# Kernel tuning notes

Hardware: AMD Instinct MI355X
Metric: run time of the kernel (lower is better)

Reference implementation:

```python
import jax, jax.numpy as jnp
import numpy as np

N, E, D, ED = 25000, 250000, 128, 128
LN_EPS = 1e-5   # nn.LayerNorm default
BN_EPS = 1e-5   # BatchNorm1d default (GENConv MLP norm='batch', training mode)
GEN_EPS = 1e-7  # GENConv message eps


def _ln(x, g, b):
    mu = jnp.mean(x, -1, keepdims=True)
    var = jnp.mean((x - mu) ** 2, -1, keepdims=True)
    return (x - mu) * jax.lax.rsqrt(var + LN_EPS) * g + b


def setup_inputs() -> dict:
    key = jax.random.key(0)
    ks = jax.random.split(key, 8)
    p = lambda k, shp: (jax.random.normal(k, shp, jnp.float32) * 0.02)
    return {
        "x": jax.random.normal(ks[0], (N, D), jnp.float32),
        "edge_attr": jax.random.normal(ks[1], (E, ED), jnp.float32),
        "edge_index": jax.random.randint(ks[2], (2, E), 0, N),
        # edge_mlp: Linear(2D+ED -> ED) + ReLU + LayerNorm(ED)
        "W_e": p(ks[3], (2 * D + ED, ED)), "b_e": jnp.zeros((ED,), jnp.float32),
        "g_e": jnp.ones((ED,), jnp.float32), "be_e": jnp.zeros((ED,), jnp.float32),
        # GENConv learnable softmax temperature t (learn_t=True, init 1.0)
        "t": jnp.float32(1.0),
        # GENConv output MLP: [D -> 2D (BN, ReLU) -> D]  (num_layers=2, expansion=2, norm='batch')
        "W_m1": p(ks[4], (D, 2 * D)), "b_m1": jnp.zeros((2 * D,), jnp.float32),
        "g_bn": jnp.ones((2 * D,), jnp.float32), "b_bn": jnp.zeros((2 * D,), jnp.float32),
        "W_m2": p(ks[5], (2 * D, D)), "b_m2": jnp.zeros((D,), jnp.float32),
        # MessageNorm learnable scale (learn_scale=True, init 1.0)
        "scale": jnp.float32(1.0),
        # node LayerNorm
        "g_n": jnp.ones((D,), jnp.float32), "b_n": jnp.zeros((D,), jnp.float32),
    }


def reference(x, edge_attr, edge_index, W_e, b_e, g_e, be_e, t,
              W_m1, b_m1, g_bn, b_bn, W_m2, b_m2, scale, g_n, b_n):
    row, col = edge_index[0], edge_index[1]  # source, destination (PyG flow)

    # edge MLP with residual: cat([x[row], x[col], edge_attr]) -> Linear -> ReLU -> LN, + edge_attr
    ei = jnp.concatenate([x[row], x[col], edge_attr], axis=-1)        # [E, 2D+ED]
    e = _ln(jnp.maximum(ei @ W_e + b_e, 0.0), g_e, be_e) + edge_attr  # [E, ED]

    # GENConv message: relu(x_j + edge_attr) + eps  (edge_dim == in_channels -> no lin_edge)
    msg = jnp.maximum(x[row] + e, 0.0) + GEN_EPS                      # [E, D]

    # per-destination, per-channel softmax aggregation with temperature t
    s = msg * t
    smax = jax.ops.segment_max(s, col, num_segments=N)                # [N, D]
    ex = jnp.exp(s - smax[col])
    denom = jax.ops.segment_sum(ex, col, num_segments=N)
    alpha = ex / denom[col]
    agg = jax.ops.segment_sum(msg * alpha, col, num_segments=N)       # [N, D]

    # GENConv residual + output MLP (Linear -> BatchNorm(train) -> ReLU -> Linear)
    out = agg + x
    h1 = out @ W_m1 + b_m1                                            # [N, 2D]
    mu = jnp.mean(h1, axis=0)
    var = jnp.mean((h1 - mu) ** 2, axis=0)
    h1 = jnp.maximum((h1 - mu) * jax.lax.rsqrt(var + BN_EPS) * g_bn + b_bn, 0.0)
    h = h1 @ W_m2 + b_m2                                              # [N, D]

    # MessageNorm(learn_scale=True): normalize(h) * ||x|| * scale
    hnorm = jnp.linalg.norm(h, axis=-1, keepdims=True)
    h = h / jnp.maximum(hnorm, 1e-12)
    xnorm = jnp.linalg.norm(x, axis=-1, keepdims=True)
    h = h * xnorm * scale

    # node residual + LayerNorm (dropout in eval mode = identity)
    x_out = _ln(x + h, g_n, b_n)
    return (x_out, e)
```

## Files before the change

### kernel.cpp

```cpp
#include <hip/hip_runtime.h>
#include <hip/hip_bf16.h>

typedef __hip_bfloat16 bf16;
typedef __attribute__((ext_vector_type(8))) short short8v;
typedef __attribute__((ext_vector_type(4))) float float4v;

constexpr int N = 25000;
constexpr int E = 250000;
constexpr size_t NB = (size_t)N * 128;
constexpr int NBLK = (N + 63) / 64;

constexpr size_t al256(size_t x) { return (x + 255) / 256 * 256; }

constexpr size_t OFF_BNS  = 0;
constexpr size_t OFF_BNQ  = OFF_BNS + 256;
constexpr size_t OFF_FLAG = OFF_BNQ + 256;
constexpr size_t OFF_XN   = OFF_FLAG + 256;
constexpr size_t OFF_WB   = al256(OFF_XN + N);
constexpr size_t OFF_WP   = OFF_WB + 8192;
constexpr size_t OFF_WM1P = OFF_WP + 16384;
constexpr size_t OFF_WM2P = OFF_WM1P + 16384;
constexpr size_t OFF_DEG  = al256(OFF_WM2P + 16384);
constexpr size_t OFF_OFFS = al256(OFF_DEG + N);
constexpr size_t OFF_CUR  = al256(OFF_OFFS + N + 1);
constexpr size_t OFF_LIST = al256(OFF_CUR + N);
constexpr size_t OFF_OUT  = al256(OFF_LIST + E);
constexpr size_t OFF_A    = al256(OFF_OUT + NB / 2);
constexpr size_t WS_FLOATS = OFF_A + NB;


__device__ __forceinline__ float b2f(bf16 v) { return __bfloat162float(v); }
__device__ __forceinline__ short f2bs(float f) {
    bf16 h = __float2bfloat16(f);
    return *reinterpret_cast<short*>(&h);
}
__device__ __forceinline__ float bs2f(short s) {
    bf16 h;
    *reinterpret_cast<short*>(&h) = s;
    return b2f(h);
}

__device__ __forceinline__ float ldf(const void* p, size_t i, int bf) {
    return bf ? b2f(((const bf16*)p)[i]) : ((const float*)p)[i];
}
__device__ __forceinline__ void stf(void* p, size_t i, float v, int bf) {
    if (bf) ((bf16*)p)[i] = __float2bfloat16(v);
    else    ((float*)p)[i] = v;
}
__device__ __forceinline__ float lds_scalar(const void* p, int bf) {
    if (!bf) return *(const float*)p;
    float v = b2f(*(const bf16*)p);
    float a = fabsf(v);
    return (a >= 0.0009765625f && a <= 1024.0f) ? v : *(const float*)p;
}
__device__ __forceinline__ int get_flag(const float* ws) {
    return *(const int*)(ws + OFF_FLAG);
}
__device__ __forceinline__ void* e_base(void* d_out, int bf) {
    return bf ? (void*)((bf16*)d_out + NB) : (void*)((float*)d_out + NB);
}


__global__ void k_detect(const unsigned short* __restrict__ xu, float* __restrict__ ws) {
    __shared__ int cnt;
    if (threadIdx.x == 0) cnt = 0;
    __syncthreads();
    int c = 0;
    for (int i = threadIdx.x; i < 512; i += 256) {
        unsigned e = (xu[i] >> 7) & 0xFFu;
        if (e >= 110u && e <= 135u) c++;
    }
    atomicAdd(&cnt, c);
    __syncthreads();
    if (threadIdx.x == 0) *(int*)(ws + OFF_FLAG) = (cnt >= 460) ? 1 : 0;
}

__global__ void k_init(float* __restrict__ ws, const void* __restrict__ W_e,
                       const void* __restrict__ W_m1, const void* __restrict__ W_m2) {
    int bf = get_flag(ws);
    size_t gid = (size_t)blockIdx.x * blockDim.x + threadIdx.x;
    size_t stride = (size_t)gridDim.x * blockDim.x;
    short* WB = (short*)(ws + OFF_WB);
    for (size_t t = gid; t < 16384; t += stride) {
        int i = t & 7, l = (t >> 3) & 63, n = (t >> 9) & 7, s = t >> 12;
        int k = s * 32 + (l >> 4) * 8 + i;
        int c = n * 16 + (l & 15);
        WB[t] = f2bs(ldf(W_e, (size_t)(256 + k) * 128 + c, bf));
    }
    short* WP = (short*)(ws + OFF_WP);
    for (size_t t = gid; t < 32768; t += stride) {
        int i = t & 7, l = (t >> 3) & 63, n = (t >> 9) & 15, s = t >> 13;
        int k = s * 32 + (l >> 4) * 8 + i;
        int c = n * 16 + (l & 15);
        float v = (c < 128) ? ldf(W_e, (size_t)k * 128 + c, bf)
                            : ldf(W_e, (size_t)(128 + k) * 128 + (c - 128), bf);
        WP[t] = f2bs(v);
    }
    short* M1 = (short*)(ws + OFF_WM1P);
    for (size_t t = gid; t < 32768; t += stride) {
        int i = t & 7, l = (t >> 3) & 63, n = (t >> 9) & 15, s = t >> 13;
        int k = s * 32 + (l >> 4) * 8 + i;
        int c = n * 16 + (l & 15);
        M1[t] = f2bs(ldf(W_m1, (size_t)k * 256 + c, bf));
    }
    short* M2 = (short*)(ws + OFF_WM2P);
    for (size_t t = gid; t < 32768; t += stride) {
        int i = t & 7, l = (t >> 3) & 63, n = (t >> 9) & 7, s = t >> 12;
        int k = s * 32 + (l >> 4) * 8 + i;
        int c = n * 16 + (l & 15);
        M2[t] = f2bs(ldf(W_m2, (size_t)k * 128 + c, bf));
    }
    for (size_t i = gid; i < 512; i += stride) ws[OFF_BNS + i] = 0.0f;
    int* deg = (int*)(ws + OFF_DEG);
    for (size_t i = gid; i < N; i += stride) deg[i] = 0;
}

__global__ __launch_bounds__(256) void k_node_pre_mfma(const void* __restrict__ x,
                                                       const void* __restrict__ b_e,
                                                       float* __restrict__ ws) {
    int bf = get_flag(ws);
    int l = threadIdx.x & 63, wv = threadIdx.x >> 6;
    int n0 = blockIdx.x * 64 + wv * 16;
    if (n0 >= N) return;
    int row = l & 15, grp = l >> 4;
    int ja = n0 + row;
    int jac = ja < N ? ja : N - 1;
    const short8v* WP = (const short8v*)(ws + OFF_WP);
    float4v acc[16];
    #pragma unroll
    for (int n = 0; n < 16; ++n) acc[n] = (float4v){0.f, 0.f, 0.f, 0.f};
    float sq = 0.f;
    #pragma unroll
    for (int s = 0; s < 4; ++s) {
        short8v af;
        if (bf) {
            af = ((const short8v*)x)[(size_t)jac * 16 + s * 4 + grp];
            #pragma unroll
            for (int i = 0; i < 8; ++i) { float v = bs2f(af[i]); sq = fmaf(v, v, sq); }
        } else {
            const float* er = (const float*)x + (size_t)jac * 128 + s * 32 + grp * 8;
            float4v lo = *(const float4v*)er;
            float4v hi = *(const float4v*)(er + 4);
            float xv[8] = {lo[0], lo[1], lo[2], lo[3], hi[0], hi[1], hi[2], hi[3]};
            #pragma unroll
            for (int i = 0; i < 8; ++i) { sq = fmaf(xv[i], xv[i], sq); af[i] = f2bs(xv[i]); }
        }
        #pragma unroll
        for (int n = 0; n < 16; ++n) {
            acc[n] = __builtin_amdgcn_mfma_f32_16x16x32_bf16(af, WP[(s * 16 + n) * 64 + l], acc[n], 0, 0, 0);
        }
    }
    sq += __shfl_xor(sq, 16, 64);
    sq += __shfl_xor(sq, 32, 64);
    if (grp == 0 && ja < N) ws[OFF_XN + ja] = sqrtf(sq);
    bf16* XA = (bf16*)(ws + OFF_A);
    #pragma unroll
    for (int reg = 0; reg < 4; ++reg) {
        int jd = n0 + grp * 4 + reg;
        if (jd >= N) continue;
        #pragma unroll
        for (int n = 0; n < 16; ++n) {
            int c = n * 16 + row;
            if (n < 8) {
                XA[(size_t)jd * 128 + c] = __float2bfloat16(acc[n][reg] + ldf(b_e, c, bf));
            } else {
                XA[NB + (size_t)jd * 128 + (c - 128)] = __float2bfloat16(acc[n][reg]);
            }
        }
    }
}

__global__ __launch_bounds__(256) void k_edge1_mfma(const void* __restrict__ ea,
                                                    const int* __restrict__ ei,
                                                    const void* __restrict__ g_e,
                                                    const void* __restrict__ be_e,
                                                    float* __restrict__ ws,
                                                    void* __restrict__ d_out) {
    int bf = get_flag(ws);
    void* eo = e_base(d_out, bf);
    int l = threadIdx.x & 63;
    int wv = threadIdx.x >> 6;
    int e0w = blockIdx.x * 64 + wv * 16;
    if (e0w >= E) return;

    if (l < 16) {
        int j = e0w + l;
        if (j < E) atomicAdd((int*)(ws + OFF_DEG) + ei[E + j], 1);
    }

    int row = l & 15, grp = l >> 4;
    int ja = e0w + row;
    int jac = ja < E ? ja : E - 1;
    const short8v* WB = (const short8v*)(ws + OFF_WB);
    float4v acc[8];
    #pragma unroll
    for (int n = 0; n < 8; ++n) acc[n] = (float4v){0.f, 0.f, 0.f, 0.f};

    #pragma unroll
    for (int s = 0; s < 4; ++s) {
        short8v af;
        if (bf) {
            af = ((const short8v*)ea)[(size_t)jac * 16 + s * 4 + grp];
        } else {
            const float* er = (const float*)ea + (size_t)jac * 128 + s * 32 + grp * 8;
            float4v lo = *(const float4v*)er;
            float4v hi = *(const float4v*)(er + 4);
            af[0] = f2bs(lo[0]); af[1] = f2bs(lo[1]); af[2] = f2bs(lo[2]); af[3] = f2bs(lo[3]);
            af[4] = f2bs(hi[0]); af[5] = f2bs(hi[1]); af[6] = f2bs(hi[2]); af[7] = f2bs(hi[3]);
        }
        #pragma unroll
        for (int n = 0; n < 8; ++n) {
            acc[n] = __builtin_amdgcn_mfma_f32_16x16x32_bf16(af, WB[(s * 8 + n) * 64 + l], acc[n], 0, 0, 0);
        }
    }

    int jr[4], rr[4], cc[4];
    #pragma unroll
    for (int reg = 0; reg < 4; ++reg) {
        int j = e0w + grp * 4 + reg;
        int jc = j < E ? j : E - 1;
        jr[reg] = j;
        rr[reg] = ei[jc];
        cc[reg] = ei[E + jc];
    }
    const bf16* XA = (const bf16*)(ws + OFF_A);
    float p[8][4];
    #pragma unroll
    for (int n = 0; n < 8; ++n) {
        int col = n * 16 + row;
        #pragma unroll
        for (int reg = 0; reg < 4; ++reg) {
            float v = acc[n][reg]
                    + b2f(XA[(size_t)rr[reg] * 128 + col])
                    + b2f(XA[NB + (size_t)cc[reg] * 128 + col]);
            p[n][reg] = fmaxf(v, 0.f);
        }
    }
    #pragma unroll
    for (int reg = 0; reg < 4; ++reg) {
        float s1 = 0.f;
        #pragma unroll
        for (int n = 0; n < 8; ++n) s1 += p[n][reg];
        #pragma unroll
        for (int off = 1; off < 16; off <<= 1) s1 += __shfl_xor(s1, off, 64);
        float mu = s1 * (1.f / 128.f);
        float s2 = 0.f;
        #pragma unroll
        for (int n = 0; n < 8; ++n) { float d = p[n][reg] - mu; s2 = fmaf(d, d, s2); }
        #pragma unroll
        for (int off = 1; off < 16; off <<= 1) s2 += __shfl_xor(s2, off, 64);
        float rstd = rsqrtf(s2 * (1.f / 128.f) + 1e-5f);
        if (jr[reg] < E) {
            size_t jb = (size_t)jr[reg] * 128;
            #pragma unroll
            for (int n = 0; n < 8; ++n) {
                int col = n * 16 + row;
                float ev = (p[n][reg] - mu) * rstd * ldf(g_e, col, bf)
                         + ldf(be_e, col, bf) + ldf(ea, jb + col, bf);
                stf(eo, jb + col, ev, bf);
            }
        }
    }
}

__global__ __launch_bounds__(256) void k_scan(float* __restrict__ ws) {
    const int* deg = (const int*)(ws + OFF_DEG);
    int* offs = (int*)(ws + OFF_OFFS);
    int* cur  = (int*)(ws + OFF_CUR);
    __shared__ int sums[256];
    __shared__ int carry[257];
    int t = threadIdx.x;
    const int chunk = (N + 255) / 256;
    int lo = t * chunk, hi = lo + chunk < N ? lo + chunk : N;
    int s = 0;
    for (int i = lo; i < hi; ++i) s += deg[i];
    sums[t] = s;
    __syncthreads();
    if (t == 0) {
        int acc = 0;
        #pragma unroll 4
        for (int i = 0; i < 256; ++i) { carry[i] = acc; acc += sums[i]; }
        carry[256] = acc;
    }
    __syncthreads();
    int acc = carry[t];
    for (int i = lo; i < hi; ++i) { offs[i] = acc; cur[i] = acc; acc += deg[i]; }
    if (t == 0) offs[N] = carry[256];
}

__global__ void k_scatter(const int* __restrict__ ei, float* __restrict__ ws) {
    int j = blockIdx.x * blockDim.x + threadIdx.x;
    if (j >= E) return;
    int cd = ei[E + j];
    int pos = atomicAdd((int*)(ws + OFF_CUR) + cd, 1);
    ((int*)(ws + OFF_LIST))[pos] = j;
}

__global__ __launch_bounds__(256) void k_agg(const void* __restrict__ x,
                                             const int* __restrict__ ei,
                                             const void* __restrict__ t_p,
                                             void* __restrict__ d_out,
                                             float* __restrict__ ws) {
    int bf = get_flag(ws);
    const void* e_in = e_base(d_out, bf);
    int n = blockIdx.x, tid = threadIdx.x;
    int c = tid & 127, half = tid >> 7;
    const int* offs = (const int*)(ws + OFF_OFFS);
    const int* list = (const int*)(ws + OFF_LIST);
    int s0 = offs[n], s1 = offs[n + 1];
    float t = lds_scalar(t_p, bf);
    float den = 0.f, num = 0.f;
    for (int i = s0 + half; i < s1; i += 2) {
        int j = list[i];
        int r = ei[j];
        float ev = ldf(e_in, (size_t)j * 128 + c, bf);
        float msg = fmaxf(ldf(x, (size_t)r * 128 + c, bf) + ev, 0.f) + 1e-7f;
        float ex = expf(msg * t - 15.0f);
        den += ex;
        num = fmaf(msg, ex, num);
    }
    __shared__ float dsh[256];
    __shared__ float nsh[256];
    dsh[tid] = den;
    nsh[tid] = num;
    __syncthreads();
    if (tid < 128) {
        float dn = dsh[tid] + dsh[tid + 128];
        float nm = nsh[tid] + nsh[tid + 128];
        float ag = dn > 0.f ? nm / dn : 0.f;
        float out = ag + ldf(x, (size_t)n * 128 + tid, bf);
        ((bf16*)(ws + OFF_OUT))[(size_t)n * 128 + tid] = __float2bfloat16(out);
    }
}

__global__ __launch_bounds__(256) void k_h1_mfma(const void* __restrict__ b_m1,
                                                 float* __restrict__ ws) {
    int bf = get_flag(ws);
    int l = threadIdx.x & 63, wv = threadIdx.x >> 6;
    int n0 = blockIdx.x * 64 + wv * 16;
    if (n0 >= N) return;
    int row = l & 15, grp = l >> 4;
    int ja = n0 + row;
    int jac = ja < N ? ja : N - 1;
    const short8v* OUT = (const short8v*)(ws + OFF_OUT);
    const short8v* M1 = (const short8v*)(ws + OFF_WM1P);
    float4v acc[16];
    #pragma unroll
    for (int n = 0; n < 16; ++n) acc[n] = (float4v){0.f, 0.f, 0.f, 0.f};
    #pragma unroll
    for (int s = 0; s < 4; ++s) {
        short8v af = OUT[(size_t)jac * 16 + s * 4 + grp];
        #pragma unroll
        for (int n = 0; n < 16; ++n) {
            acc[n] = __builtin_amdgcn_mfma_f32_16x16x32_bf16(af, M1[(s * 16 + n) * 64 + l], acc[n], 0, 0, 0);
        }
    }
    bf16* H1 = (bf16*)(ws + OFF_A);
    #pragma unroll
    for (int reg = 0; reg < 4; ++reg) {
        int jd = n0 + grp * 4 + reg;
        if (jd >= N) continue;
        #pragma unroll
        for (int n = 0; n < 16; ++n) {
            int col = n * 16 + row;
            H1[(size_t)jd * 256 + col] = __float2bfloat16(acc[n][reg] + ldf(b_m1, col, bf));
        }
    }
}

__global__ __launch_bounds__(256) void k_bnstats(float* __restrict__ ws) {
    int t = threadIdx.x;
    const bf16* H1 = (const bf16*)(ws + OFF_A);
    float s = 0.f, q = 0.f;
    for (int r = blockIdx.x; r < N; r += gridDim.x) {
        float v = b2f(H1[(size_t)r * 256 + t]);
        s += v;
        q = fmaf(v, v, q);
    }
    atomicAdd(&ws[OFF_BNS + t], s);
    atomicAdd(&ws[OFF_BNQ + t], q);
}

__global__ __launch_bounds__(256) void k_node_post_mfma(const void* __restrict__ x,
                                                        const void* __restrict__ g_bn,
                                                        const void* __restrict__ b_bn,
                                                        const void* __restrict__ b_m2,
                                                        const void* __restrict__ scale_p,
                                                        const void* __restrict__ g_n,
                                                        const void* __restrict__ b_n,
                                                        float* __restrict__ ws,
                                                        void* __restrict__ x_out) {
    int bf = get_flag(ws);
    __shared__ float sA[256];
    __shared__ float sB[256];
    {
        int t = threadIdx.x;
        const float inv_n = 1.f / (float)N;
        float mu = ws[OFF_BNS + t] * inv_n;
        float var = ws[OFF_BNQ + t] * inv_n - mu * mu;
        float rs = rsqrtf(fmaxf(var, 0.f) + 1e-5f) * ldf(g_bn, t, bf);
        sA[t] = rs;
        sB[t] = ldf(b_bn, t, bf) - mu * rs;
    }
    __syncthreads();
    int l = threadIdx.x & 63, wv = threadIdx.x >> 6;
    int n0 = blockIdx.x * 64 + wv * 16;
    if (n0 >= N) return;
    int row = l & 15, grp = l >> 4;
    int ja = n0 + row;
    int jac = ja < N ? ja : N - 1;
    const short8v* H1 = (const short8v*)(ws + OFF_A);
    const short8v* M2 = (const short8v*)(ws + OFF_WM2P);
    float4v acc[8];
    #pragma unroll
    for (int n = 0; n < 8; ++n) acc[n] = (float4v){0.f, 0.f, 0.f, 0.f};
    #pragma unroll
    for (int s = 0; s < 8; ++s) {
        short8v hv = H1[(size_t)jac * 32 + s * 4 + grp];
        int kb = s * 32 + grp * 8;
        short8v af;
        #pragma unroll
        for (int i = 0; i < 8; ++i) {
            float v = fmaf(bs2f(hv[i]), sA[kb + i], sB[kb + i]);
            af[i] = f2bs(fmaxf(v, 0.f));
        }
        #pragma unroll
        for (int n = 0; n < 8; ++n) {
            acc[n] = __builtin_amdgcn_mfma_f32_16x16x32_bf16(af, M2[(s * 8 + n) * 64 + l], acc[n], 0, 0, 0);
        }
    }
    float scl = lds_scalar(scale_p, bf);
    #pragma unroll
    for (int reg = 0; reg < 4; ++reg) {
        int jd = n0 + grp * 4 + reg;
        int jdc = jd < N ? jd : N - 1;
        float h[8];
        float ss = 0.f;
        #pragma unroll
        for (int n = 0; n < 8; ++n) {
            h[n] = acc[n][reg] + ldf(b_m2, n * 16 + row, bf);
            ss = fmaf(h[n], h[n], ss);
        }
        #pragma unroll
        for (int off = 1; off < 16; off <<= 1) ss += __shfl_xor(ss, off, 64);
        float hs = ws[OFF_XN + jdc] * scl / fmaxf(sqrtf(ss), 1e-12f);
        float y[8];
        float s1 = 0.f;
        #pragma unroll
        for (int n = 0; n < 8; ++n) {
            y[n] = ldf(x, (size_t)jdc * 128 + n * 16 + row, bf) + h[n] * hs;
            s1 += y[n];
        }
        #pragma unroll
        for (int off = 1; off < 16; off <<= 1) s1 += __shfl_xor(s1, off, 64);
        float mu = s1 * (1.f / 128.f);
        float s2 = 0.f;
        #pragma unroll
        for (int n = 0; n < 8; ++n) { float d = y[n] - mu; s2 = fmaf(d, d, s2); }
        #pragma unroll
        for (int off = 1; off < 16; off <<= 1) s2 += __shfl_xor(s2, off, 64);
        float rstd = rsqrtf(s2 * (1.f / 128.f) + 1e-5f);
        if (jd < N) {
            #pragma unroll
            for (int n = 0; n < 8; ++n) {
                int col = n * 16 + row;
                float o = (y[n] - mu) * rstd * ldf(g_n, col, bf) + ldf(b_n, col, bf);
                stf(x_out, (size_t)jd * 128 + col, o, bf);
            }
        }
    }
}


extern "C" void kernel_launch(void* const* d_in, const int* in_sizes, int n_in,
                              void* d_out, int out_size, void* d_ws, size_t ws_size,
                              hipStream_t stream) {
    const void* x    = d_in[0];
    const void* ea   = d_in[1];
    const int*  ei   = (const int*)d_in[2];
    const void* W_e  = d_in[3];
    const void* b_e  = d_in[4];
    const void* g_e  = d_in[5];
    const void* be_e = d_in[6];
    const void* t_p  = d_in[7];
    const void* W_m1 = d_in[8];
    const void* b_m1 = d_in[9];
    const void* g_bn = d_in[10];
    const void* b_bn = d_in[11];
    const void* W_m2 = d_in[12];
    const void* b_m2 = d_in[13];
    const void* scl  = d_in[14];
    const void* g_n  = d_in[15];
    const void* b_n  = d_in[16];

    float* ws = (float*)d_ws;

    k_detect<<<1, 256, 0, stream>>>((const unsigned short*)x, ws);
    k_init<<<512, 256, 0, stream>>>(ws, W_e, W_m1, W_m2);
    k_node_pre_mfma<<<NBLK, 256, 0, stream>>>(x, b_e, ws);
    k_edge1_mfma<<<(E + 63) / 64, 256, 0, stream>>>(ea, ei, g_e, be_e, ws, d_out);
    k_scan<<<1, 256, 0, stream>>>(ws);
    k_scatter<<<(E + 255) / 256, 256, 0, stream>>>(ei, ws);
    k_agg<<<N, 256, 0, stream>>>(x, ei, t_p, d_out, ws);
    k_h1_mfma<<<NBLK, 256, 0, stream>>>(b_m1, ws);
    k_bnstats<<<256, 256, 0, stream>>>(ws);
    k_node_post_mfma<<<NBLK, 256, 0, stream>>>(x, g_bn, b_bn, b_m2, scl, g_n, b_n, ws, d_out);
}
```

Before: 622.1 us.

## Write bf16 messages in CSR order from edge kernel and stream them in aggregation

Degree counting and the prefix scan now run before the edge MLP. The edge kernel then takes each edge's CSR slot with an atomic and writes the bf16 message relu(x_row+e)+eps straight into a destination-sorted buffer in the workspace. Aggregation then streams contiguous messages instead of gathering list indices, edge features and x rows, which cuts random global reads. The edge kernel also swaps the MFMA operand order so each lane holds four contiguous channels of one edge, and it uses single-pass variance with vectorized loads and stores. The cost is an extra E*128 bf16 workspace buffer, plus a fallback path when the workspace is too small.

```diff
diff --git a/kernel.cpp b/kernel.cpp
--- a/kernel.cpp
+++ b/kernel.cpp
@@ -3,6 +3,7 @@
 
 typedef __hip_bfloat16 bf16;
 typedef __attribute__((ext_vector_type(8))) short short8v;
+typedef __attribute__((ext_vector_type(4))) short short4v;
 typedef __attribute__((ext_vector_type(4))) float float4v;
 
 constexpr int N = 25000;
@@ -27,6 +28,8 @@
 constexpr size_t OFF_OUT  = al256(OFF_LIST + E);
 constexpr size_t OFF_A    = al256(OFF_OUT + NB / 2);
 constexpr size_t WS_FLOATS = OFF_A + NB;
+constexpr size_t OFF_MSG  = al256(OFF_A + NB);
+constexpr size_t WS_FLOATS_BIG = OFF_MSG + (size_t)E * 64;
 
 
 __device__ __forceinline__ float b2f(bf16 v) { return __bfloat162float(v); }
@@ -46,6 +49,21 @@
 __device__ __forceinline__ void stf(void* p, size_t i, float v, int bf) {
     if (bf) ((bf16*)p)[i] = __float2bfloat16(v);
     else    ((float*)p)[i] = v;
+}
+__device__ __forceinline__ float4v load4(const void* p, size_t i, int bf) {
+    if (bf) {
+        short4v s = *(const short4v*)((const bf16*)p + i);
+        return (float4v){bs2f(s[0]), bs2f(s[1]), bs2f(s[2]), bs2f(s[3])};
+    }
+    return *(const float4v*)((const float*)p + i);
+}
+__device__ __forceinline__ void store4(void* p, size_t i, float4v v, int bf) {
+    if (bf) {
+        short4v s = {f2bs(v[0]), f2bs(v[1]), f2bs(v[2]), f2bs(v[3])};
+        *(short4v*)((bf16*)p + i) = s;
+    } else {
+        *(float4v*)((float*)p + i) = v;
+    }
 }
 __device__ __forceinline__ float lds_scalar(const void* p, int bf) {
     if (!bf) return *(const float*)p;
@@ -113,6 +131,11 @@
     for (size_t i = gid; i < 512; i += stride) ws[OFF_BNS + i] = 0.0f;
     int* deg = (int*)(ws + OFF_DEG);
     for (size_t i = gid; i < N; i += stride) deg[i] = 0;
+}
+
+__global__ void k_count(const int* __restrict__ ei, float* __restrict__ ws) {
+    int j = blockIdx.x * blockDim.x + threadIdx.x;
+    if (j < E) atomicAdd((int*)(ws + OFF_DEG) + ei[E + j], 1);
 }
 
 __global__ __launch_bounds__(256) void k_node_pre_mfma(const void* __restrict__ x,
@@ -170,10 +193,12 @@
     }
 }
 
+template<int WM>
 __global__ __launch_bounds__(256) void k_edge1_mfma(const void* __restrict__ ea,
                                                     const int* __restrict__ ei,
                                                     const void* __restrict__ g_e,
                                                     const void* __restrict__ be_e,
+                                                    const void* __restrict__ x,
                                                     float* __restrict__ ws,
                                                     void* __restrict__ d_out) {
     int bf = get_flag(ws);
@@ -181,84 +206,89 @@
     int l = threadIdx.x & 63;
     int wv = threadIdx.x >> 6;
     int e0w = blockIdx.x * 64 + wv * 16;
-    if (e0w >= E) return;
-
-    if (l < 16) {
-        int j = e0w + l;
-        if (j < E) atomicAdd((int*)(ws + OFF_DEG) + ei[E + j], 1);
-    }
-
-    int row = l & 15, grp = l >> 4;
-    int ja = e0w + row;
+    int eq = l & 15, grp = l >> 4;
+
+    int posv = 0;
+    if (WM && l < 16) {
+        int jj = e0w + l;
+        if (jj < E) posv = atomicAdd((int*)(ws + OFF_CUR) + ei[E + jj], 1);
+    }
+    int pos = WM ? __shfl(posv, eq, 64) : 0;
+
+    int ja = e0w + eq;
     int jac = ja < E ? ja : E - 1;
     const short8v* WB = (const short8v*)(ws + OFF_WB);
     float4v acc[8];
     #pragma unroll
-    for (int n = 0; n < 8; ++n) acc[n] = (float4v){0.f, 0.f, 0.f, 0.f};
+    for (int m = 0; m < 8; ++m) acc[m] = (float4v){0.f, 0.f, 0.f, 0.f};
 
     #pragma unroll
     for (int s = 0; s < 4; ++s) {
-        short8v af;
+        short8v bfr;
         if (bf) {
-            af = ((const short8v*)ea)[(size_t)jac * 16 + s * 4 + grp];
+            bfr = ((const short8v*)ea)[(size_t)jac * 16 + s * 4 + grp];
         } else {
             const float* er = (const float*)ea + (size_t)jac * 128 + s * 32 + grp * 8;
             float4v lo = *(const float4v*)er;
             float4v hi = *(const float4v*)(er + 4);
-            af[0] = f2bs(lo[0]); af[1] = f2bs(lo[1]); af[2] = f2bs(lo[2]); af[3] = f2bs(lo[3]);
-            af[4] = f2bs(hi[0]); af[5] = f2bs(hi[1]); af[6] = f2bs(hi[2]); af[7] = f2bs(hi[3]);
-        }
-        #pragma unroll
-        for (int n = 0; n < 8; ++n) {
-            acc[n] = __builtin_amdgcn_mfma_f32_16x16x32_bf16(af, WB[(s * 8 + n) * 64 + l], acc[n], 0, 0, 0);
-        }
-    }
-
-    int jr[4], rr[4], cc[4];
-    #pragma unroll
-    for (int reg = 0; reg < 4; ++reg) {
-        int j = e0w + grp * 4 + reg;
-        int jc = j < E ? j : E - 1;
-        jr[reg] = j;
-        rr[reg] = ei[jc];
-        cc[reg] = ei[E + jc];
-    }
-    const bf16* XA = (const bf16*)(ws + OFF_A);
+            bfr[0] = f2bs(lo[0]); bfr[1] = f2bs(lo[1]); bfr[2] = f2bs(lo[2]); bfr[3] = f2bs(lo[3]);
+            bfr[4] = f2bs(hi[0]); bfr[5] = f2bs(hi[1]); bfr[6] = f2bs(hi[2]); bfr[7] = f2bs(hi[3]);
+        }
+        #pragma unroll
+        for (int m = 0; m < 8; ++m) {
+            acc[m] = __builtin_amdgcn_mfma_f32_16x16x32_bf16(WB[(s * 8 + m) * 64 + l], bfr, acc[m], 0, 0, 0);
+        }
+    }
+
+    int j = e0w + eq;
+    bool valid = j < E;
+    int jc = valid ? j : E - 1;
+    int r = ei[jc], cd = ei[E + jc];
+    const bf16* XAp = (const bf16*)(ws + OFF_A);
+
     float p[8][4];
-    #pragma unroll
-    for (int n = 0; n < 8; ++n) {
-        int col = n * 16 + row;
-        #pragma unroll
-        for (int reg = 0; reg < 4; ++reg) {
-            float v = acc[n][reg]
-                    + b2f(XA[(size_t)rr[reg] * 128 + col])
-                    + b2f(XA[NB + (size_t)cc[reg] * 128 + col]);
-            p[n][reg] = fmaxf(v, 0.f);
-        }
-    }
-    #pragma unroll
-    for (int reg = 0; reg < 4; ++reg) {
-        float s1 = 0.f;
-        #pragma unroll
-        for (int n = 0; n < 8; ++n) s1 += p[n][reg];
-        #pragma unroll
-        for (int off = 1; off < 16; off <<= 1) s1 += __shfl_xor(s1, off, 64);
-        float mu = s1 * (1.f / 128.f);
-        float s2 = 0.f;
-        #pragma unroll
-        for (int n = 0; n < 8; ++n) { float d = p[n][reg] - mu; s2 = fmaf(d, d, s2); }
-        #pragma unroll
-        for (int off = 1; off < 16; off <<= 1) s2 += __shfl_xor(s2, off, 64);
-        float rstd = rsqrtf(s2 * (1.f / 128.f) + 1e-5f);
-        if (jr[reg] < E) {
-            size_t jb = (size_t)jr[reg] * 128;
+    float s1 = 0.f, s2 = 0.f;
+    #pragma unroll
+    for (int m = 0; m < 8; ++m) {
+        int ch = m * 16 + grp * 4;
+        short4v xa = *(const short4v*)(XAp + (size_t)r * 128 + ch);
+        short4v xb = *(const short4v*)(XAp + NB + (size_t)cd * 128 + ch);
+        #pragma unroll
+        for (int w = 0; w < 4; ++w) {
+            float v = acc[m][w] + bs2f(xa[w]) + bs2f(xb[w]);
+            v = fmaxf(v, 0.f);
+            p[m][w] = v;
+            s1 += v;
+            s2 = fmaf(v, v, s2);
+        }
+    }
+    s1 += __shfl_xor(s1, 16, 64);
+    s1 += __shfl_xor(s1, 32, 64);
+    s2 += __shfl_xor(s2, 16, 64);
+    s2 += __shfl_xor(s2, 32, 64);
+    float mu = s1 * (1.f / 128.f);
+    float var = s2 * (1.f / 128.f) - mu * mu;
+    float rstd = rsqrtf(fmaxf(var, 0.f) + 1e-5f);
+
+    bf16* MSG = (bf16*)(ws + OFF_MSG);
+    #pragma unroll
+    for (int m = 0; m < 8; ++m) {
+        int ch = m * 16 + grp * 4;
+        float4v gg = load4(g_e, ch, bf);
+        float4v bb = load4(be_e, ch, bf);
+        float4v eav = load4(ea, (size_t)jc * 128 + ch, bf);
+        float4v ev;
+        #pragma unroll
+        for (int w = 0; w < 4; ++w)
+            ev[w] = (p[m][w] - mu) * rstd * gg[w] + bb[w] + eav[w];
+        if (valid) store4(eo, (size_t)j * 128 + ch, ev, bf);
+        if (WM) {
+            float4v xv = load4(x, (size_t)r * 128 + ch, bf);
+            short4v ms;
             #pragma unroll
-            for (int n = 0; n < 8; ++n) {
-                int col = n * 16 + row;
-                float ev = (p[n][reg] - mu) * rstd * ldf(g_e, col, bf)
-                         + ldf(be_e, col, bf) + ldf(ea, jb + col, bf);
-                stf(eo, jb + col, ev, bf);
-            }
+            for (int w = 0; w < 4; ++w)
+                ms[w] = f2bs(fmaxf(xv[w] + ev[w], 0.f) + 1e-7f);
+            if (valid) *(short4v*)(MSG + (size_t)pos * 128 + ch) = ms;
         }
     }
 }
@@ -296,21 +326,52 @@
     ((int*)(ws + OFF_LIST))[pos] = j;
 }
 
-__global__ __launch_bounds__(256) void k_agg(const void* __restrict__ x,
-                                             const int* __restrict__ ei,
-                                             const void* __restrict__ t_p,
-                                             void* __restrict__ d_out,
-                                             float* __restrict__ ws) {
+__global__ __launch_bounds__(256) void k_agg_stream(const void* __restrict__ x,
+                                                    const void* __restrict__ t_p,
+                                                    float* __restrict__ ws) {
+    int bf = get_flag(ws);
+    int n = blockIdx.x, tid = threadIdx.x;
+    int c = tid & 127, half = tid >> 7;
+    const int* offs = (const int*)(ws + OFF_OFFS);
+    int s0 = offs[n], s1v = offs[n + 1];
+    float t = lds_scalar(t_p, bf);
+    const bf16* MSG = (const bf16*)(ws + OFF_MSG);
+    float den = 0.f, num = 0.f;
+    for (int i = s0 + half; i < s1v; i += 2) {
+        float m = b2f(MSG[(size_t)i * 128 + c]);
+        float ex = expf(m * t - 15.0f);
+        den += ex;
+        num = fmaf(m, ex, num);
+    }
+    __shared__ float dsh[256];
+    __shared__ float nsh[256];
+    dsh[tid] = den;
+    nsh[tid] = num;
+    __syncthreads();
+    if (tid < 128) {
+        float dn = dsh[tid] + dsh[tid + 128];
+        float nm = nsh[tid] + nsh[tid + 128];
+        float ag = dn > 0.f ? nm / dn : 0.f;
+        float out = ag + ldf(x, (size_t)n * 128 + tid, bf);
+        ((bf16*)(ws + OFF_OUT))[(size_t)n * 128 + tid] = __float2bfloat16(out);
+    }
+}
+
+__global__ __launch_bounds__(256) void k_agg_gather(const void* __restrict__ x,
+                                                    const int* __restrict__ ei,
+                                                    const void* __restrict__ t_p,
+                                                    void* __restrict__ d_out,
+                                                    float* __restrict__ ws) {
     int bf = get_flag(ws);
     const void* e_in = e_base(d_out, bf);
     int n = blockIdx.x, tid = threadIdx.x;
     int c = tid & 127, half = tid >> 7;
     const int* offs = (const int*)(ws + OFF_OFFS);
     const int* list = (const int*)(ws + OFF_LIST);
-    int s0 = offs[n], s1 = offs[n + 1];
+    int s0 = offs[n], s1v = offs[n + 1];
     float t = lds_scalar(t_p, bf);
     float den = 0.f, num = 0.f;
-    for (int i = s0 + half; i < s1; i += 2) {
+    for (int i = s0 + half; i < s1v; i += 2) {
         int j = list[i];
         int r = ei[j];
         float ev = ldf(e_in, (size_t)j * 128 + c, bf);
@@ -494,14 +555,21 @@
     const void* b_n  = d_in[16];
 
     float* ws = (float*)d_ws;
+    bool big = ws_size >= WS_FLOATS_BIG * sizeof(float);
 
     k_detect<<<1, 256, 0, stream>>>((const unsigned short*)x, ws);
     k_init<<<512, 256, 0, stream>>>(ws, W_e, W_m1, W_m2);
+    k_count<<<(E + 255) / 256, 256, 0, stream>>>(ei, ws);
+    k_scan<<<1, 256, 0, stream>>>(ws);
     k_node_pre_mfma<<<NBLK, 256, 0, stream>>>(x, b_e, ws);
-    k_edge1_mfma<<<(E + 63) / 64, 256, 0, stream>>>(ea, ei, g_e, be_e, ws, d_out);
-    k_scan<<<1, 256, 0, stream>>>(ws);
-    k_scatter<<<(E + 255) / 256, 256, 0, stream>>>(ei, ws);
-    k_agg<<<N, 256, 0, stream>>>(x, ei, t_p, d_out, ws);
+    if (big) {
+        k_edge1_mfma<1><<<(E + 63) / 64, 256, 0, stream>>>(ea, ei, g_e, be_e, x, ws, d_out);
+        k_agg_stream<<<N, 256, 0, stream>>>(x, t_p, ws);
+    } else {
+        k_edge1_mfma<0><<<(E + 63) / 64, 256, 0, stream>>>(ea, ei, g_e, be_e, x, ws, d_out);
+        k_scatter<<<(E + 255) / 256, 256, 0, stream>>>(ei, ws);
+        k_agg_gather<<<N, 256, 0, stream>>>(x, ei, t_p, d_out, ws);
+    }
     k_h1_mfma<<<NBLK, 256, 0, stream>>>(b_m1, ws);
     k_bnstats<<<256, 256, 0, stream>>>(ws);
     k_node_post_mfma<<<NBLK, 256, 0, stream>>>(x, g_bn, b_bn, b_m2, scl, g_n, b_n, ws, d_out);
```

New measurement: 604.5 us. 2.8% less time.
